# Performance work log

Hardware: AMD Instinct MI355X
Metric: run time of the kernel (lower is better)

The kernel has to match this reference:

```python
import jax, jax.numpy as jnp
import numpy as np

D_MODEL = 1024
D_FF = 4096
NUM_EXPERTS = 8
TOP_K = 2


def setup_inputs() -> dict:
    key = jax.random.key(0)
    ks = jax.random.split(key, 9)
    s = 0.02
    x = jax.random.normal(ks[0], (2, 2048, D_MODEL), dtype=jnp.float32)
    Wg = jax.random.normal(ks[1], (D_MODEL, NUM_EXPERTS), dtype=jnp.float32) * s
    bg = jnp.zeros((NUM_EXPERTS,), dtype=jnp.float32)
    W1 = jax.random.normal(ks[2], (NUM_EXPERTS, D_MODEL, D_FF), dtype=jnp.float32) * s
    b1 = jnp.zeros((NUM_EXPERTS, D_FF), dtype=jnp.float32)
    W3 = jax.random.normal(ks[3], (NUM_EXPERTS, D_MODEL, D_FF), dtype=jnp.float32) * s
    b3 = jnp.zeros((NUM_EXPERTS, D_FF), dtype=jnp.float32)
    W2 = jax.random.normal(ks[4], (NUM_EXPERTS, D_FF, D_MODEL), dtype=jnp.float32) * s
    b2 = jnp.zeros((NUM_EXPERTS, D_MODEL), dtype=jnp.float32)
    return {"x": x, "Wg": Wg, "bg": bg, "W1": W1, "b1": b1,
            "W3": W3, "b3": b3, "W2": W2, "b2": b2}


def reference(x, Wg, bg, W1, b1, W3, b3, W2, b2):
    # Gate (eval mode: no gaussian noise, no dropout)
    logits = x @ Wg + bg                                  # [b, s, E]
    probs = jax.nn.softmax(logits, axis=-1)
    top_v, top_i = jax.lax.top_k(probs, TOP_K)            # [b, s, K]
    top_v = top_v / (top_v.sum(axis=-1, keepdims=True) + 1e-6)
    # combine[b,s,e] = sum_k top_v[b,s,k] * 1[top_i[b,s,k]==e]
    onehot = jax.nn.one_hot(top_i, NUM_EXPERTS, dtype=x.dtype)  # [b, s, K, E]
    combine = jnp.einsum('bsk,bske->bse', top_v, onehot)        # [b, s, E]

    out = jnp.zeros_like(x)
    for e in range(NUM_EXPERTS):
        # SwiGLU expert FFN applied densely; masked-out tokens zeroed by combine weight
        h = jax.nn.silu(x @ W1[e] + b1[e]) * (x @ W3[e] + b3[e])   # [b, s, d_ff]
        out = out + combine[..., e:e + 1] * (h @ W2[e] + b2[e])
    return out
```

## Files before the change

kernel.cpp:

```cpp
#include <hip/hip_runtime.h>
#include <stdint.h>

#define D_MODEL 1024
#define D_FF    4096
#define NE      8
#define T_TOK   4096
#define R_TOT   8192

typedef float f32x4 __attribute__((ext_vector_type(4)));
typedef __bf16 bf16x8 __attribute__((ext_vector_type(8)));
typedef unsigned short ushort_t;

__device__ __forceinline__ ushort_t f2bf(float f) {
    unsigned int u = __float_as_uint(f);
    u += 0x7FFFu + ((u >> 16) & 1u);
    return (ushort_t)(u >> 16);
}

__device__ __forceinline__ void async16(const void* g, const void* l) {
    __builtin_amdgcn_global_load_lds(
        (const __attribute__((address_space(1))) unsigned int*)(uintptr_t)g,
        (__attribute__((address_space(3))) unsigned int*)(uintptr_t)l,
        16, 0, 0);
}

__global__ __launch_bounds__(256) void k_gate(
    const float* __restrict__ x, const float* __restrict__ Wg, const float* __restrict__ bg,
    int* __restrict__ topi, float* __restrict__ topw, int* __restrict__ counts)
{
    int wave = threadIdx.x >> 6, lane = threadIdx.x & 63;
    int t = blockIdx.x * 4 + wave;
    const float* xr = x + (size_t)t * D_MODEL;
    float acc[NE];
#pragma unroll
    for (int e = 0; e < NE; ++e) acc[e] = 0.f;
#pragma unroll
    for (int i = 0; i < D_MODEL / 64; ++i) {
        int k = i * 64 + lane;
        float xv = xr[k];
        const float4* wgp = (const float4*)(Wg + (size_t)k * NE);
        float4 w0 = wgp[0], w1 = wgp[1];
        acc[0] += xv * w0.x; acc[1] += xv * w0.y; acc[2] += xv * w0.z; acc[3] += xv * w0.w;
        acc[4] += xv * w1.x; acc[5] += xv * w1.y; acc[6] += xv * w1.z; acc[7] += xv * w1.w;
    }
#pragma unroll
    for (int off = 32; off >= 1; off >>= 1)
#pragma unroll
        for (int e = 0; e < NE; ++e) acc[e] += __shfl_down(acc[e], off, 64);
    if (lane == 0) {
        float l[NE], m = -1e30f;
#pragma unroll
        for (int e = 0; e < NE; ++e) { l[e] = acc[e] + bg[e]; m = fmaxf(m, l[e]); }
        float p[NE], Z = 0.f;
#pragma unroll
        for (int e = 0; e < NE; ++e) { p[e] = __expf(l[e] - m); Z += p[e]; }
        float invZ = 1.f / Z;
        int i0 = 0; float v0 = -1.f;
#pragma unroll
        for (int e = 0; e < NE; ++e) { p[e] *= invZ; if (p[e] > v0) { v0 = p[e]; i0 = e; } }
        int i1 = 0; float v1 = -1.f;
#pragma unroll
        for (int e = 0; e < NE; ++e) { if (e != i0 && p[e] > v1) { v1 = p[e]; i1 = e; } }
        float denom = 1.f / (v0 + v1 + 1e-6f);
        topi[t * 2 + 0] = i0; topi[t * 2 + 1] = i1;
        topw[t * 2 + 0] = v0 * denom; topw[t * 2 + 1] = v1 * denom;
        atomicAdd(&counts[i0], 1); atomicAdd(&counts[i1], 1);
    }
}

__global__ void k_scan(const int* __restrict__ counts, int* __restrict__ offsets,
                       int* __restrict__ cursors)
{
    if (threadIdx.x == 0) {
        int acc = 0;
        for (int e = 0; e < NE; ++e) { offsets[e] = acc; cursors[e] = acc; acc += counts[e]; }
    }
}

__global__ __launch_bounds__(256) void k_scatter(
    const int* __restrict__ topi, const float* __restrict__ topw,
    int* __restrict__ cursors, int* __restrict__ btok, float* __restrict__ bw)
{
    int t = blockIdx.x * 256 + threadIdx.x;
#pragma unroll
    for (int k = 0; k < 2; ++k) {
        int e = topi[t * 2 + k];
        int p = atomicAdd(&cursors[e], 1);
        btok[p] = t;
        bw[p] = topw[t * 2 + k];
    }
}

__global__ __launch_bounds__(256) void k_gather(
    const float* __restrict__ x, const int* __restrict__ btok, ushort_t* __restrict__ Xg)
{
    int i = blockIdx.x;
    int t = btok[i];
    float4 v = ((const float4*)(x + (size_t)t * D_MODEL))[threadIdx.x];
    ushort4 o;
    o.x = f2bf(v.x); o.y = f2bf(v.y); o.z = f2bf(v.z); o.w = f2bf(v.w);
    ((ushort4*)(Xg + (size_t)i * D_MODEL))[threadIdx.x] = o;
}

__global__ __launch_bounds__(256) void k_transpose(
    const float* __restrict__ W, ushort_t* __restrict__ Wt, int K, int N)
{
    __shared__ ushort_t tile[64 * 72];
    int e = blockIdx.z;
    const float* We = W + (size_t)e * K * N;
    ushort_t* Wte = Wt + (size_t)e * K * N;
    int nb = blockIdx.x * 64, kb = blockIdx.y * 64;
    int tn4 = (threadIdx.x & 15) * 4;
    int tk = threadIdx.x >> 4;
#pragma unroll
    for (int r = 0; r < 4; ++r) {
        int k = r * 16 + tk;
        float4 v = *(const float4*)(We + (size_t)(kb + k) * N + nb + tn4);
        tile[(tn4 + 0) * 72 + k] = f2bf(v.x);
        tile[(tn4 + 1) * 72 + k] = f2bf(v.y);
        tile[(tn4 + 2) * 72 + k] = f2bf(v.z);
        tile[(tn4 + 3) * 72 + k] = f2bf(v.w);
    }
    __syncthreads();
#pragma unroll
    for (int c = 0; c < 4; ++c) {
        int chunk = c * 256 + threadIdx.x;
        int n = chunk >> 4, kc = (chunk & 15) * 4;
        ushort4 o = *(const ushort4*)&tile[n * 72 + kc];
        *(ushort4*)(Wte + (size_t)(nb + n) * K + kb + kc) = o;
    }
}


__global__ __launch_bounds__(512, 2) void k_gemm1(
    const ushort_t* __restrict__ Xg, const ushort_t* __restrict__ W1t,
    const ushort_t* __restrict__ W3t,
    const float* __restrict__ b1, const float* __restrict__ b3,
    const int* __restrict__ counts, const int* __restrict__ offsets,
    ushort_t* __restrict__ H)
{
    __shared__ __align__(16) ushort_t sA [2][256 * 64];
    __shared__ __align__(16) ushort_t sB1[2][128 * 64];
    __shared__ __align__(16) ushort_t sB3[2][128 * 64];

    int bx = blockIdx.x;
    int lx = (bx & 7) * 5 + (bx >> 3);

    int tm = lx, e = 0, cnt = 0;
    for (; e < NE; ++e) {
        cnt = counts[e];
        int nt = (cnt + 255) >> 8;
        if (tm < nt) break;
        tm -= nt;
    }
    if (e >= NE) return;
    int row0 = offsets[e] + tm * 256;
    int rows_left = cnt - tm * 256;

    int tile_n = blockIdx.y * 128;
    int tid = threadIdx.x, wave = tid >> 6, lane = tid & 63;
    int wm = (wave >> 1) * 64, wn = (wave & 1) * 64;
    int col = lane & 15, quad = lane >> 4;

    const ushort_t* W1e = W1t + (size_t)e * D_FF * D_MODEL;
    const ushort_t* W3e = W3t + (size_t)e * D_FF * D_MODEL;

    const ushort_t* gA[4]; const ushort_t* gB1[2]; const ushort_t* gB3[2];
    unsigned offA[4], offB[2];
#pragma unroll
    for (int s = 0; s < 4; ++s) {
        int q = (wave * 4 + s) * 64 + lane;
        int r = q >> 3;
        int cg = ((q & 7) ^ (r & 7)) * 8;
        gA[s]  = Xg + (size_t)(row0 + r) * D_MODEL + cg;
        offA[s] = (unsigned)(wave * 4 + s) * 512;
    }
#pragma unroll
    for (int s = 0; s < 2; ++s) {
        int q = (wave * 2 + s) * 64 + lane;
        int r = q >> 3;
        int cg = ((q & 7) ^ (r & 7)) * 8;
        gB1[s] = W1e + (size_t)(tile_n + r) * D_MODEL + cg;
        gB3[s] = W3e + (size_t)(tile_n + r) * D_MODEL + cg;
        offB[s] = (unsigned)(wave * 2 + s) * 512;
    }

    int swz = (quad ^ (col & 7)) * 8;
    unsigned fA[4], fB[4];
#pragma unroll
    for (int i = 0; i < 4; ++i) {
        fA[i] = (unsigned)(wm + i * 16 + col) * 64 + swz;
        fB[i] = (unsigned)(wn + i * 16 + col) * 64 + swz;
    }

    f32x4 acc1[4][4], acc3[4][4];
#pragma unroll
    for (int i = 0; i < 4; ++i)
#pragma unroll
        for (int j = 0; j < 4; ++j) {
            acc1[i][j] = (f32x4){0.f, 0.f, 0.f, 0.f};
            acc3[i][j] = (f32x4){0.f, 0.f, 0.f, 0.f};
        }

#define STAGE1(p, k0)                                                          \
    do {                                                                       \
        _Pragma("unroll")                                                      \
        for (int s_ = 0; s_ < 4; ++s_) async16(gA[s_] + (k0), &sA[p][offA[s_]]); \
        _Pragma("unroll")                                                      \
        for (int s_ = 0; s_ < 2; ++s_) {                                       \
            async16(gB1[s_] + (k0), &sB1[p][offB[s_]]);                        \
            async16(gB3[s_] + (k0), &sB3[p][offB[s_]]);                        \
        }                                                                      \
    } while (0)

    STAGE1(0, 0);
    for (int t = 0; t < D_MODEL / 64; ++t) {
        int p = t & 1;
        if (t < D_MODEL / 64 - 1) {
            STAGE1(p ^ 1, (t + 1) * 64);
            asm volatile("s_waitcnt vmcnt(8)" ::: "memory");
        } else {
            asm volatile("s_waitcnt vmcnt(0)" ::: "memory");
        }
        __builtin_amdgcn_s_barrier();
        asm volatile("" ::: "memory");
#pragma unroll
        for (int kk = 0; kk < 2; ++kk) {
            unsigned kx = kk * 32;
            bf16x8 a[4], u1[4], u3[4];
#pragma unroll
            for (int j = 0; j < 4; ++j) {
                u1[j] = *(const bf16x8*)(&sB1[p][fB[j] ^ kx]);
                u3[j] = *(const bf16x8*)(&sB3[p][fB[j] ^ kx]);
            }
#pragma unroll
            for (int i = 0; i < 4; ++i) a[i] = *(const bf16x8*)(&sA[p][fA[i] ^ kx]);
            __builtin_amdgcn_s_setprio(1);
#pragma unroll
            for (int i = 0; i < 4; ++i)
#pragma unroll
                for (int j = 0; j < 4; ++j) {
                    acc1[i][j] = __builtin_amdgcn_mfma_f32_16x16x32_bf16(a[i], u1[j], acc1[i][j], 0, 0, 0);
                    acc3[i][j] = __builtin_amdgcn_mfma_f32_16x16x32_bf16(a[i], u3[j], acc3[i][j], 0, 0, 0);
                }
            __builtin_amdgcn_s_setprio(0);
        }
        asm volatile("" ::: "memory");
        __builtin_amdgcn_s_barrier();
        asm volatile("" ::: "memory");
    }
#undef STAGE1

#pragma unroll
    for (int j = 0; j < 4; ++j) {
        int n = tile_n + wn + j * 16 + col;
        float bias1 = b1[e * D_FF + n];
        float bias3 = b3[e * D_FF + n];
#pragma unroll
        for (int i = 0; i < 4; ++i) {
            int rbase = wm + i * 16 + quad * 4;
#pragma unroll
            for (int r = 0; r < 4; ++r) {
                int row = rbase + r;
                if (row < rows_left) {
                    float h1 = acc1[i][j][r] + bias1;
                    float h3 = acc3[i][j][r] + bias3;
                    float s = h1 / (1.f + __expf(-h1));
                    H[(size_t)(row0 + row) * D_FF + n] = f2bf(s * h3);
                }
            }
        }
    }
}

__global__ __launch_bounds__(512, 2) void k_gemm2(
    const ushort_t* __restrict__ H, const ushort_t* __restrict__ W2t,
    const float* __restrict__ b2,
    const int* __restrict__ counts, const int* __restrict__ offsets,
    const int* __restrict__ btok, const float* __restrict__ bw,
    float* __restrict__ out)
{
    __shared__ __align__(16) ushort_t sA[2][256 * 64];
    __shared__ __align__(16) ushort_t sB[2][128 * 64];

    int bx = blockIdx.x;
    int lx = (bx & 7) * 5 + (bx >> 3);

    int tm = lx, e = 0, cnt = 0;
    for (; e < NE; ++e) {
        cnt = counts[e];
        int nt = (cnt + 255) >> 8;
        if (tm < nt) break;
        tm -= nt;
    }
    if (e >= NE) return;
    int row0 = offsets[e] + tm * 256;
    int rows_left = cnt - tm * 256;

    int tile_n = blockIdx.y * 128;
    int tid = threadIdx.x, wave = tid >> 6, lane = tid & 63;
    int wm = (wave >> 1) * 64, wn = (wave & 1) * 64;
    int col = lane & 15, quad = lane >> 4;

    const ushort_t* W2e = W2t + (size_t)e * D_MODEL * D_FF;

    const ushort_t* gA[4]; const ushort_t* gB[2];
    unsigned offA[4], offB[2];
#pragma unroll
    for (int s = 0; s < 4; ++s) {
        int q = (wave * 4 + s) * 64 + lane;
        int r = q >> 3;
        int cg = ((q & 7) ^ (r & 7)) * 8;
        gA[s] = H + (size_t)(row0 + r) * D_FF + cg;
        offA[s] = (unsigned)(wave * 4 + s) * 512;
    }
#pragma unroll
    for (int s = 0; s < 2; ++s) {
        int q = (wave * 2 + s) * 64 + lane;
        int r = q >> 3;
        int cg = ((q & 7) ^ (r & 7)) * 8;
        gB[s] = W2e + (size_t)(tile_n + r) * D_FF + cg;
        offB[s] = (unsigned)(wave * 2 + s) * 512;
    }

    int swz = (quad ^ (col & 7)) * 8;
    unsigned fA[4], fB[4];
#pragma unroll
    for (int i = 0; i < 4; ++i) {
        fA[i] = (unsigned)(wm + i * 16 + col) * 64 + swz;
        fB[i] = (unsigned)(wn + i * 16 + col) * 64 + swz;
    }

    f32x4 acc[4][4];
#pragma unroll
    for (int i = 0; i < 4; ++i)
#pragma unroll
        for (int j = 0; j < 4; ++j) acc[i][j] = (f32x4){0.f, 0.f, 0.f, 0.f};

#define STAGE2(p, k0)                                                          \
    do {                                                                       \
        _Pragma("unroll")                                                      \
        for (int s_ = 0; s_ < 4; ++s_) async16(gA[s_] + (k0), &sA[p][offA[s_]]); \
        _Pragma("unroll")                                                      \
        for (int s_ = 0; s_ < 2; ++s_) async16(gB[s_] + (k0), &sB[p][offB[s_]]); \
    } while (0)

    STAGE2(0, 0);
    for (int t = 0; t < D_FF / 64; ++t) {
        int p = t & 1;
        if (t < D_FF / 64 - 1) {
            STAGE2(p ^ 1, (t + 1) * 64);
            asm volatile("s_waitcnt vmcnt(6)" ::: "memory");
        } else {
            asm volatile("s_waitcnt vmcnt(0)" ::: "memory");
        }
        __builtin_amdgcn_s_barrier();
        asm volatile("" ::: "memory");
#pragma unroll
        for (int kk = 0; kk < 2; ++kk) {
            unsigned kx = kk * 32;
            bf16x8 a[4], b[4];
#pragma unroll
            for (int j = 0; j < 4; ++j) b[j] = *(const bf16x8*)(&sB[p][fB[j] ^ kx]);
#pragma unroll
            for (int i = 0; i < 4; ++i) a[i] = *(const bf16x8*)(&sA[p][fA[i] ^ kx]);
            __builtin_amdgcn_s_setprio(1);
#pragma unroll
            for (int i = 0; i < 4; ++i)
#pragma unroll
                for (int j = 0; j < 4; ++j)
                    acc[i][j] = __builtin_amdgcn_mfma_f32_16x16x32_bf16(a[i], b[j], acc[i][j], 0, 0, 0);
            __builtin_amdgcn_s_setprio(0);
        }
        asm volatile("" ::: "memory");
        __builtin_amdgcn_s_barrier();
        asm volatile("" ::: "memory");
    }
#undef STAGE2

    float bias[4];
#pragma unroll
    for (int j = 0; j < 4; ++j) bias[j] = b2[e * D_MODEL + tile_n + wn + j * 16 + col];

#pragma unroll
    for (int i = 0; i < 4; ++i) {
        int rbase = wm + i * 16 + quad * 4;
#pragma unroll
        for (int r = 0; r < 4; ++r) {
            int row = rbase + r;
            if (row < rows_left) {
                int g_r = row0 + row;
                int t = btok[g_r];
                float w = bw[g_r];
                float* orow = out + (size_t)t * D_MODEL + tile_n + wn + col;
#pragma unroll
                for (int j = 0; j < 4; ++j)
                    atomicAdd(orow + j * 16, w * (acc[i][j][r] + bias[j]));
            }
        }
    }
}

extern "C" void kernel_launch(void* const* d_in, const int* in_sizes, int n_in,
                              void* d_out, int out_size, void* d_ws, size_t ws_size,
                              hipStream_t stream)
{
    const float* x  = (const float*)d_in[0];
    const float* Wg = (const float*)d_in[1];
    const float* bg = (const float*)d_in[2];
    const float* W1 = (const float*)d_in[3];
    const float* b1 = (const float*)d_in[4];
    const float* W3 = (const float*)d_in[5];
    const float* b3 = (const float*)d_in[6];
    const float* W2 = (const float*)d_in[7];
    const float* b2 = (const float*)d_in[8];
    float* out = (float*)d_out;

    char* ws = (char*)d_ws;
    int*   counts  = (int*)(ws + 0);
    int*   cursors = (int*)(ws + 32);
    int*   offsets = (int*)(ws + 64);
    int*   topi    = (int*)(ws + 256);
    float* topw    = (float*)(ws + 256 + 32768);
    int*   btok    = (int*)(ws + 256 + 65536);
    float* bw      = (float*)(ws + 256 + 98304);
    char* p = ws + 131328;
    ushort_t* Xg  = (ushort_t*)p;  p += (size_t)R_TOT * D_MODEL * 2;
    ushort_t* Hb  = (ushort_t*)p;  p += (size_t)R_TOT * D_FF * 2;
    ushort_t* W1t = (ushort_t*)p;  p += (size_t)NE * D_FF * D_MODEL * 2;
    ushort_t* W3t = (ushort_t*)p;  p += (size_t)NE * D_FF * D_MODEL * 2;
    ushort_t* W2t = (ushort_t*)p;

    hipMemsetAsync(ws, 0, 64, stream);
    hipMemsetAsync(d_out, 0, (size_t)out_size * 4, stream);

    k_gate<<<dim3(T_TOK / 4), dim3(256), 0, stream>>>(x, Wg, bg, topi, topw, counts);
    k_scan<<<dim3(1), dim3(64), 0, stream>>>(counts, offsets, cursors);
    k_scatter<<<dim3(T_TOK / 256), dim3(256), 0, stream>>>(topi, topw, cursors, btok, bw);
    k_gather<<<dim3(R_TOT), dim3(256), 0, stream>>>(x, btok, Xg);
    k_transpose<<<dim3(D_FF / 64, D_MODEL / 64, NE), dim3(256), 0, stream>>>(W1, W1t, D_MODEL, D_FF);
    k_transpose<<<dim3(D_FF / 64, D_MODEL / 64, NE), dim3(256), 0, stream>>>(W3, W3t, D_MODEL, D_FF);
    k_transpose<<<dim3(D_MODEL / 64, D_FF / 64, NE), dim3(256), 0, stream>>>(W2, W2t, D_FF, D_MODEL);
    k_gemm1<<<dim3(40, D_FF / 128), dim3(512), 0, stream>>>(Xg, W1t, W3t, b1, b3, counts, offsets, Hb);
    k_gemm2<<<dim3(40, D_MODEL / 128), dim3(512), 0, stream>>>(Hb, W2t, b2, counts, offsets, btok, bw, out);
}
```

Before: 914.6 us.

## Interleave prefetch with MFMA phases, triple-buffer gemm2, replace atomics with combine kernel

The gemm1 main loop is split into four half-K MFMA phases. Each phase issues part of the next tile's async loads, so global-to-LDS traffic overlaps with compute instead of arriving in one burst. gemm2 moves to a three-stage LDS buffer with prefetch two tiles ahead, and now writes unweighted per-slot outputs to a scratch buffer Y (aliased onto W1t) instead of doing float atomicAdds into out. A new k_combine kernel gathers the two expert rows per token using positions recorded by k_scatter. This removes the output memset and atomic contention, at the cost of more barriers, more LDS per block (possible occupancy loss) and an extra pass over Y.

```diff
diff --git a/kernel.cpp b/kernel.cpp
--- a/kernel.cpp
+++ b/kernel.cpp
@@ -23,6 +23,8 @@
         (__attribute__((address_space(3))) unsigned int*)(uintptr_t)l,
         16, 0, 0);
 }
+
+#define FENCE() asm volatile("" ::: "memory")
 
 __global__ __launch_bounds__(256) void k_gate(
     const float* __restrict__ x, const float* __restrict__ Wg, const float* __restrict__ bg,
@@ -78,16 +80,18 @@
 }
 
 __global__ __launch_bounds__(256) void k_scatter(
-    const int* __restrict__ topi, const float* __restrict__ topw,
+    const int* __restrict__ topi_in, const float* __restrict__ topw,
     int* __restrict__ cursors, int* __restrict__ btok, float* __restrict__ bw)
 {
     int t = blockIdx.x * 256 + threadIdx.x;
+    int* topi = (int*)topi_in;
 #pragma unroll
     for (int k = 0; k < 2; ++k) {
         int e = topi[t * 2 + k];
         int p = atomicAdd(&cursors[e], 1);
         btok[p] = t;
         bw[p] = topw[t * 2 + k];
+        topi[t * 2 + k] = p;
     }
 }
 
@@ -202,54 +206,106 @@
             acc3[i][j] = (f32x4){0.f, 0.f, 0.f, 0.f};
         }
 
-#define STAGE1(p, k0)                                                          \
-    do {                                                                       \
-        _Pragma("unroll")                                                      \
-        for (int s_ = 0; s_ < 4; ++s_) async16(gA[s_] + (k0), &sA[p][offA[s_]]); \
-        _Pragma("unroll")                                                      \
-        for (int s_ = 0; s_ < 2; ++s_) {                                       \
-            async16(gB1[s_] + (k0), &sB1[p][offB[s_]]);                        \
-            async16(gB3[s_] + (k0), &sB3[p][offB[s_]]);                        \
-        }                                                                      \
-    } while (0)
-
-    STAGE1(0, 0);
+#pragma unroll
+    for (int s = 0; s < 4; ++s) async16(gA[s], &sA[0][offA[s]]);
+#pragma unroll
+    for (int s = 0; s < 2; ++s) async16(gB1[s], &sB1[0][offB[s]]);
+#pragma unroll
+    for (int s = 0; s < 2; ++s) async16(gB3[s], &sB3[0][offB[s]]);
+    asm volatile("s_waitcnt vmcnt(2)" ::: "memory");
+    __builtin_amdgcn_s_barrier();
+    FENCE();
+
     for (int t = 0; t < D_MODEL / 64; ++t) {
         int p = t & 1;
-        if (t < D_MODEL / 64 - 1) {
-            STAGE1(p ^ 1, (t + 1) * 64);
-            asm volatile("s_waitcnt vmcnt(8)" ::: "memory");
+        int k1 = (t + 1) * 64;
+        bool pf = (t < D_MODEL / 64 - 1);
+        bf16x8 a[4], u[4];
+
+#pragma unroll
+        for (int i = 0; i < 4; ++i) a[i] = *(const bf16x8*)(&sA[p][fA[i]]);
+#pragma unroll
+        for (int j = 0; j < 4; ++j) u[j] = *(const bf16x8*)(&sB1[p][fB[j]]);
+        if (pf) {
+            async16(gA[0] + k1, &sA[p ^ 1][offA[0]]);
+            async16(gA[1] + k1, &sA[p ^ 1][offA[1]]);
+            asm volatile("s_waitcnt vmcnt(2)" ::: "memory");
         } else {
             asm volatile("s_waitcnt vmcnt(0)" ::: "memory");
         }
         __builtin_amdgcn_s_barrier();
-        asm volatile("" ::: "memory");
-#pragma unroll
-        for (int kk = 0; kk < 2; ++kk) {
-            unsigned kx = kk * 32;
-            bf16x8 a[4], u1[4], u3[4];
-#pragma unroll
-            for (int j = 0; j < 4; ++j) {
-                u1[j] = *(const bf16x8*)(&sB1[p][fB[j] ^ kx]);
-                u3[j] = *(const bf16x8*)(&sB3[p][fB[j] ^ kx]);
-            }
-#pragma unroll
-            for (int i = 0; i < 4; ++i) a[i] = *(const bf16x8*)(&sA[p][fA[i] ^ kx]);
-            __builtin_amdgcn_s_setprio(1);
-#pragma unroll
-            for (int i = 0; i < 4; ++i)
-#pragma unroll
-                for (int j = 0; j < 4; ++j) {
-                    acc1[i][j] = __builtin_amdgcn_mfma_f32_16x16x32_bf16(a[i], u1[j], acc1[i][j], 0, 0, 0);
-                    acc3[i][j] = __builtin_amdgcn_mfma_f32_16x16x32_bf16(a[i], u3[j], acc3[i][j], 0, 0, 0);
-                }
-            __builtin_amdgcn_s_setprio(0);
-        }
-        asm volatile("" ::: "memory");
-        __builtin_amdgcn_s_barrier();
-        asm volatile("" ::: "memory");
-    }
-#undef STAGE1
+        FENCE();
+        __builtin_amdgcn_s_setprio(1);
+#pragma unroll
+        for (int i = 0; i < 4; ++i)
+#pragma unroll
+            for (int j = 0; j < 4; ++j)
+                acc1[i][j] = __builtin_amdgcn_mfma_f32_16x16x32_bf16(a[i], u[j], acc1[i][j], 0, 0, 0);
+        __builtin_amdgcn_s_setprio(0);
+        FENCE();
+        __builtin_amdgcn_s_barrier();
+        FENCE();
+
+#pragma unroll
+        for (int j = 0; j < 4; ++j) u[j] = *(const bf16x8*)(&sB3[p][fB[j]]);
+        if (pf) {
+            async16(gA[2] + k1, &sA[p ^ 1][offA[2]]);
+            async16(gA[3] + k1, &sA[p ^ 1][offA[3]]);
+        }
+        __builtin_amdgcn_s_barrier();
+        FENCE();
+        __builtin_amdgcn_s_setprio(1);
+#pragma unroll
+        for (int i = 0; i < 4; ++i)
+#pragma unroll
+            for (int j = 0; j < 4; ++j)
+                acc3[i][j] = __builtin_amdgcn_mfma_f32_16x16x32_bf16(a[i], u[j], acc3[i][j], 0, 0, 0);
+        __builtin_amdgcn_s_setprio(0);
+        FENCE();
+        __builtin_amdgcn_s_barrier();
+        FENCE();
+
+#pragma unroll
+        for (int i = 0; i < 4; ++i) a[i] = *(const bf16x8*)(&sA[p][fA[i] ^ 32]);
+#pragma unroll
+        for (int j = 0; j < 4; ++j) u[j] = *(const bf16x8*)(&sB1[p][fB[j] ^ 32]);
+        if (pf) {
+            async16(gB1[0] + k1, &sB1[p ^ 1][offB[0]]);
+            async16(gB1[1] + k1, &sB1[p ^ 1][offB[1]]);
+        }
+        __builtin_amdgcn_s_barrier();
+        FENCE();
+        __builtin_amdgcn_s_setprio(1);
+#pragma unroll
+        for (int i = 0; i < 4; ++i)
+#pragma unroll
+            for (int j = 0; j < 4; ++j)
+                acc1[i][j] = __builtin_amdgcn_mfma_f32_16x16x32_bf16(a[i], u[j], acc1[i][j], 0, 0, 0);
+        __builtin_amdgcn_s_setprio(0);
+        FENCE();
+        __builtin_amdgcn_s_barrier();
+        FENCE();
+
+#pragma unroll
+        for (int j = 0; j < 4; ++j) u[j] = *(const bf16x8*)(&sB3[p][fB[j] ^ 32]);
+        if (pf) {
+            async16(gB3[0] + k1, &sB3[p ^ 1][offB[0]]);
+            async16(gB3[1] + k1, &sB3[p ^ 1][offB[1]]);
+            asm volatile("s_waitcnt vmcnt(2)" ::: "memory");
+        }
+        __builtin_amdgcn_s_barrier();
+        FENCE();
+        __builtin_amdgcn_s_setprio(1);
+#pragma unroll
+        for (int i = 0; i < 4; ++i)
+#pragma unroll
+            for (int j = 0; j < 4; ++j)
+                acc3[i][j] = __builtin_amdgcn_mfma_f32_16x16x32_bf16(a[i], u[j], acc3[i][j], 0, 0, 0);
+        __builtin_amdgcn_s_setprio(0);
+        FENCE();
+        __builtin_amdgcn_s_barrier();
+        FENCE();
+    }
 
 #pragma unroll
     for (int j = 0; j < 4; ++j) {
@@ -277,11 +333,10 @@
     const ushort_t* __restrict__ H, const ushort_t* __restrict__ W2t,
     const float* __restrict__ b2,
     const int* __restrict__ counts, const int* __restrict__ offsets,
-    const int* __restrict__ btok, const float* __restrict__ bw,
-    float* __restrict__ out)
-{
-    __shared__ __align__(16) ushort_t sA[2][256 * 64];
-    __shared__ __align__(16) ushort_t sB[2][128 * 64];
+    float* __restrict__ Y)
+{
+    __shared__ __align__(16) ushort_t sA[3][256 * 64];
+    __shared__ __align__(16) ushort_t sB[3][128 * 64];
 
     int bx = blockIdx.x;
     int lx = (bx & 7) * 5 + (bx >> 3);
@@ -337,46 +392,74 @@
 #pragma unroll
         for (int j = 0; j < 4; ++j) acc[i][j] = (f32x4){0.f, 0.f, 0.f, 0.f};
 
-#define STAGE2(p, k0)                                                          \
-    do {                                                                       \
-        _Pragma("unroll")                                                      \
-        for (int s_ = 0; s_ < 4; ++s_) async16(gA[s_] + (k0), &sA[p][offA[s_]]); \
-        _Pragma("unroll")                                                      \
-        for (int s_ = 0; s_ < 2; ++s_) async16(gB[s_] + (k0), &sB[p][offB[s_]]); \
-    } while (0)
-
-    STAGE2(0, 0);
+#pragma unroll
+    for (int s = 0; s < 4; ++s) async16(gA[s], &sA[0][offA[s]]);
+#pragma unroll
+    for (int s = 0; s < 2; ++s) async16(gB[s], &sB[0][offB[s]]);
+#pragma unroll
+    for (int s = 0; s < 4; ++s) async16(gA[s] + 64, &sA[1][offA[s]]);
+#pragma unroll
+    for (int s = 0; s < 2; ++s) async16(gB[s] + 64, &sB[1][offB[s]]);
+    asm volatile("s_waitcnt vmcnt(6)" ::: "memory");
+    __builtin_amdgcn_s_barrier();
+    FENCE();
+
+    int pb = 0;
     for (int t = 0; t < D_FF / 64; ++t) {
-        int p = t & 1;
-        if (t < D_FF / 64 - 1) {
-            STAGE2(p ^ 1, (t + 1) * 64);
+        int pn = (pb == 0) ? 2 : pb - 1;
+        int k2 = (t + 2) * 64;
+        bool pf = (t < D_FF / 64 - 2);
+        bf16x8 a[4], b[4];
+
+#pragma unroll
+        for (int i = 0; i < 4; ++i) a[i] = *(const bf16x8*)(&sA[pb][fA[i]]);
+#pragma unroll
+        for (int j = 0; j < 4; ++j) b[j] = *(const bf16x8*)(&sB[pb][fB[j]]);
+        if (pf) {
+            async16(gA[0] + k2, &sA[pn][offA[0]]);
+            async16(gA[1] + k2, &sA[pn][offA[1]]);
+            async16(gA[2] + k2, &sA[pn][offA[2]]);
+        }
+        __builtin_amdgcn_s_barrier();
+        FENCE();
+        __builtin_amdgcn_s_setprio(1);
+#pragma unroll
+        for (int i = 0; i < 4; ++i)
+#pragma unroll
+            for (int j = 0; j < 4; ++j)
+                acc[i][j] = __builtin_amdgcn_mfma_f32_16x16x32_bf16(a[i], b[j], acc[i][j], 0, 0, 0);
+        __builtin_amdgcn_s_setprio(0);
+        FENCE();
+        __builtin_amdgcn_s_barrier();
+        FENCE();
+
+#pragma unroll
+        for (int i = 0; i < 4; ++i) a[i] = *(const bf16x8*)(&sA[pb][fA[i] ^ 32]);
+#pragma unroll
+        for (int j = 0; j < 4; ++j) b[j] = *(const bf16x8*)(&sB[pb][fB[j] ^ 32]);
+        if (pf) {
+            async16(gA[3] + k2, &sA[pn][offA[3]]);
+            async16(gB[0] + k2, &sB[pn][offB[0]]);
+            async16(gB[1] + k2, &sB[pn][offB[1]]);
             asm volatile("s_waitcnt vmcnt(6)" ::: "memory");
         } else {
             asm volatile("s_waitcnt vmcnt(0)" ::: "memory");
         }
         __builtin_amdgcn_s_barrier();
-        asm volatile("" ::: "memory");
-#pragma unroll
-        for (int kk = 0; kk < 2; ++kk) {
-            unsigned kx = kk * 32;
-            bf16x8 a[4], b[4];
-#pragma unroll
-            for (int j = 0; j < 4; ++j) b[j] = *(const bf16x8*)(&sB[p][fB[j] ^ kx]);
-#pragma unroll
-            for (int i = 0; i < 4; ++i) a[i] = *(const bf16x8*)(&sA[p][fA[i] ^ kx]);
-            __builtin_amdgcn_s_setprio(1);
-#pragma unroll
-            for (int i = 0; i < 4; ++i)
-#pragma unroll
-                for (int j = 0; j < 4; ++j)
-                    acc[i][j] = __builtin_amdgcn_mfma_f32_16x16x32_bf16(a[i], b[j], acc[i][j], 0, 0, 0);
-            __builtin_amdgcn_s_setprio(0);
-        }
-        asm volatile("" ::: "memory");
-        __builtin_amdgcn_s_barrier();
-        asm volatile("" ::: "memory");
-    }
-#undef STAGE2
+        FENCE();
+        __builtin_amdgcn_s_setprio(1);
+#pragma unroll
+        for (int i = 0; i < 4; ++i)
+#pragma unroll
+            for (int j = 0; j < 4; ++j)
+                acc[i][j] = __builtin_amdgcn_mfma_f32_16x16x32_bf16(a[i], b[j], acc[i][j], 0, 0, 0);
+        __builtin_amdgcn_s_setprio(0);
+        FENCE();
+        __builtin_amdgcn_s_barrier();
+        FENCE();
+
+        pb = (pb == 2) ? 0 : pb + 1;
+    }
 
     float bias[4];
 #pragma unroll
@@ -389,16 +472,30 @@
         for (int r = 0; r < 4; ++r) {
             int row = rbase + r;
             if (row < rows_left) {
-                int g_r = row0 + row;
-                int t = btok[g_r];
-                float w = bw[g_r];
-                float* orow = out + (size_t)t * D_MODEL + tile_n + wn + col;
+                float* yrow = Y + (size_t)(row0 + row) * D_MODEL + tile_n + wn + col;
 #pragma unroll
                 for (int j = 0; j < 4; ++j)
-                    atomicAdd(orow + j * 16, w * (acc[i][j][r] + bias[j]));
+                    yrow[j * 16] = acc[i][j][r] + bias[j];
             }
         }
     }
+}
+
+__global__ __launch_bounds__(256) void k_combine(
+    const float* __restrict__ Y, const int* __restrict__ pos,
+    const float* __restrict__ topw, float* __restrict__ out)
+{
+    int t = blockIdx.x, c = threadIdx.x;
+    int p0 = pos[t * 2 + 0], p1 = pos[t * 2 + 1];
+    float w0 = topw[t * 2 + 0], w1 = topw[t * 2 + 1];
+    float4 y0 = ((const float4*)(Y + (size_t)p0 * D_MODEL))[c];
+    float4 y1 = ((const float4*)(Y + (size_t)p1 * D_MODEL))[c];
+    float4 o;
+    o.x = w0 * y0.x + w1 * y1.x;
+    o.y = w0 * y0.y + w1 * y1.y;
+    o.z = w0 * y0.z + w1 * y1.z;
+    o.w = w0 * y0.w + w1 * y1.w;
+    ((float4*)(out + (size_t)t * D_MODEL))[c] = o;
 }
 
 extern "C" void kernel_launch(void* const* d_in, const int* in_sizes, int n_in,
@@ -430,9 +527,9 @@
     ushort_t* W1t = (ushort_t*)p;  p += (size_t)NE * D_FF * D_MODEL * 2;
     ushort_t* W3t = (ushort_t*)p;  p += (size_t)NE * D_FF * D_MODEL * 2;
     ushort_t* W2t = (ushort_t*)p;
+    float* Y = (float*)W1t;
 
     hipMemsetAsync(ws, 0, 64, stream);
-    hipMemsetAsync(d_out, 0, (size_t)out_size * 4, stream);
 
     k_gate<<<dim3(T_TOK / 4), dim3(256), 0, stream>>>(x, Wg, bg, topi, topw, counts);
     k_scan<<<dim3(1), dim3(64), 0, stream>>>(counts, offsets, cursors);
@@ -442,5 +539,6 @@
     k_transpose<<<dim3(D_FF / 64, D_MODEL / 64, NE), dim3(256), 0, stream>>>(W3, W3t, D_MODEL, D_FF);
     k_transpose<<<dim3(D_MODEL / 64, D_FF / 64, NE), dim3(256), 0, stream>>>(W2, W2t, D_FF, D_MODEL);
     k_gemm1<<<dim3(40, D_FF / 128), dim3(512), 0, stream>>>(Xg, W1t, W3t, b1, b3, counts, offsets, Hb);
-    k_gemm2<<<dim3(40, D_MODEL / 128), dim3(512), 0, stream>>>(Hb, W2t, b2, counts, offsets, btok, bw, out);
-}
+    k_gemm2<<<dim3(40, D_MODEL / 128), dim3(512), 0, stream>>>(Hb, W2t, b2, counts, offsets, Y);
+    k_combine<<<dim3(T_TOK), dim3(256), 0, stream>>>(Y, topi, topw, out);
+}
```

After: 894.2 us. 1.02x faster.

## Shrink GEMM tiles to 128x128x32 and replace atomic scatter with combine kernel

Applied to the files above, without the earlier changes.

Both expert GEMMs move from 256x128 tiles with 512 threads and K-step 64 to 128x128 tiles with 256 threads and K-step 32, with a new LDS swizzle and more blocks. This aims for better load balance and occupancy across CUs. The second GEMM now writes per-slot outputs to a buffer (reusing the W1t region), and a new combine kernel forms the weighted sum of each token's two expert rows. This removes the float atomics and the output memset. It costs an extra read and write of an 8192x1024 float buffer, and halving the tiles doubles global operand traffic per FLOP.

```diff
diff --git a/kernel.cpp b/kernel.cpp
--- a/kernel.cpp
+++ b/kernel.cpp
@@ -78,16 +78,18 @@
 }
 
 __global__ __launch_bounds__(256) void k_scatter(
-    const int* __restrict__ topi, const float* __restrict__ topw,
+    const int* __restrict__ topi_in, const float* __restrict__ topw,
     int* __restrict__ cursors, int* __restrict__ btok, float* __restrict__ bw)
 {
     int t = blockIdx.x * 256 + threadIdx.x;
+    int* topi = (int*)topi_in;
 #pragma unroll
     for (int k = 0; k < 2; ++k) {
         int e = topi[t * 2 + k];
         int p = atomicAdd(&cursors[e], 1);
         btok[p] = t;
         bw[p] = topw[t * 2 + k];
+        topi[t * 2 + k] = p;
     }
 }
 
@@ -105,7 +107,7 @@
 __global__ __launch_bounds__(256) void k_transpose(
     const float* __restrict__ W, ushort_t* __restrict__ Wt, int K, int N)
 {
-    __shared__ ushort_t tile[64 * 72];
+    __shared__ ushort_t tile[64 * 76];
     int e = blockIdx.z;
     const float* We = W + (size_t)e * K * N;
     ushort_t* Wte = Wt + (size_t)e * K * N;
@@ -116,46 +118,46 @@
     for (int r = 0; r < 4; ++r) {
         int k = r * 16 + tk;
         float4 v = *(const float4*)(We + (size_t)(kb + k) * N + nb + tn4);
-        tile[(tn4 + 0) * 72 + k] = f2bf(v.x);
-        tile[(tn4 + 1) * 72 + k] = f2bf(v.y);
-        tile[(tn4 + 2) * 72 + k] = f2bf(v.z);
-        tile[(tn4 + 3) * 72 + k] = f2bf(v.w);
+        tile[(tn4 + 0) * 76 + k] = f2bf(v.x);
+        tile[(tn4 + 1) * 76 + k] = f2bf(v.y);
+        tile[(tn4 + 2) * 76 + k] = f2bf(v.z);
+        tile[(tn4 + 3) * 76 + k] = f2bf(v.w);
     }
     __syncthreads();
 #pragma unroll
     for (int c = 0; c < 4; ++c) {
         int chunk = c * 256 + threadIdx.x;
         int n = chunk >> 4, kc = (chunk & 15) * 4;
-        ushort4 o = *(const ushort4*)&tile[n * 72 + kc];
+        ushort4 o = *(const ushort4*)&tile[n * 76 + kc];
         *(ushort4*)(Wte + (size_t)(nb + n) * K + kb + kc) = o;
     }
 }
 
 
-__global__ __launch_bounds__(512, 2) void k_gemm1(
+__global__ __launch_bounds__(256, 2) void k_gemm1(
     const ushort_t* __restrict__ Xg, const ushort_t* __restrict__ W1t,
     const ushort_t* __restrict__ W3t,
     const float* __restrict__ b1, const float* __restrict__ b3,
     const int* __restrict__ counts, const int* __restrict__ offsets,
     ushort_t* __restrict__ H)
 {
-    __shared__ __align__(16) ushort_t sA [2][256 * 64];
-    __shared__ __align__(16) ushort_t sB1[2][128 * 64];
-    __shared__ __align__(16) ushort_t sB3[2][128 * 64];
+    __shared__ __align__(16) ushort_t sA [2][128 * 32];
+    __shared__ __align__(16) ushort_t sB1[2][128 * 32];
+    __shared__ __align__(16) ushort_t sB3[2][128 * 32];
 
     int bx = blockIdx.x;
-    int lx = (bx & 7) * 5 + (bx >> 3);
+    int lx = (bx & 7) * 9 + (bx >> 3);
 
     int tm = lx, e = 0, cnt = 0;
     for (; e < NE; ++e) {
         cnt = counts[e];
-        int nt = (cnt + 255) >> 8;
+        int nt = (cnt + 127) >> 7;
         if (tm < nt) break;
         tm -= nt;
     }
     if (e >= NE) return;
-    int row0 = offsets[e] + tm * 256;
-    int rows_left = cnt - tm * 256;
+    int row0 = offsets[e] + tm * 128;
+    int rows_left = cnt - tm * 128;
 
     int tile_n = blockIdx.y * 128;
     int tid = threadIdx.x, wave = tid >> 6, lane = tid & 63;
@@ -165,32 +167,27 @@
     const ushort_t* W1e = W1t + (size_t)e * D_FF * D_MODEL;
     const ushort_t* W3e = W3t + (size_t)e * D_FF * D_MODEL;
 
-    const ushort_t* gA[4]; const ushort_t* gB1[2]; const ushort_t* gB3[2];
-    unsigned offA[4], offB[2];
-#pragma unroll
-    for (int s = 0; s < 4; ++s) {
-        int q = (wave * 4 + s) * 64 + lane;
-        int r = q >> 3;
-        int cg = ((q & 7) ^ (r & 7)) * 8;
-        gA[s]  = Xg + (size_t)(row0 + r) * D_MODEL + cg;
-        offA[s] = (unsigned)(wave * 4 + s) * 512;
-    }
+    const ushort_t* gA[2]; const ushort_t* gB1[2]; const ushort_t* gB3[2];
+    unsigned ldsOff[2];
 #pragma unroll
     for (int s = 0; s < 2; ++s) {
-        int q = (wave * 2 + s) * 64 + lane;
-        int r = q >> 3;
-        int cg = ((q & 7) ^ (r & 7)) * 8;
+        int u = wave * 2 + s;
+        int q = u * 64 + lane;
+        int r = q >> 2;
+        int cg = ((q & 3) ^ ((r >> 1) & 3)) * 8;
+        gA[s]  = Xg  + (size_t)(row0 + r) * D_MODEL + cg;
         gB1[s] = W1e + (size_t)(tile_n + r) * D_MODEL + cg;
         gB3[s] = W3e + (size_t)(tile_n + r) * D_MODEL + cg;
-        offB[s] = (unsigned)(wave * 2 + s) * 512;
-    }
-
-    int swz = (quad ^ (col & 7)) * 8;
+        ldsOff[s] = (unsigned)u * 512;
+    }
+
     unsigned fA[4], fB[4];
 #pragma unroll
     for (int i = 0; i < 4; ++i) {
-        fA[i] = (unsigned)(wm + i * 16 + col) * 64 + swz;
-        fB[i] = (unsigned)(wn + i * 16 + col) * 64 + swz;
+        int ra = wm + i * 16 + col;
+        int rb = wn + i * 16 + col;
+        fA[i] = (unsigned)ra * 32 + ((quad ^ ((ra >> 1) & 3)) * 8);
+        fB[i] = (unsigned)rb * 32 + ((quad ^ ((rb >> 1) & 3)) * 8);
     }
 
     f32x4 acc1[4][4], acc3[4][4];
@@ -202,49 +199,49 @@
             acc3[i][j] = (f32x4){0.f, 0.f, 0.f, 0.f};
         }
 
-#define STAGE1(p, k0)                                                          \
-    do {                                                                       \
-        _Pragma("unroll")                                                      \
-        for (int s_ = 0; s_ < 4; ++s_) async16(gA[s_] + (k0), &sA[p][offA[s_]]); \
-        _Pragma("unroll")                                                      \
-        for (int s_ = 0; s_ < 2; ++s_) {                                       \
-            async16(gB1[s_] + (k0), &sB1[p][offB[s_]]);                        \
-            async16(gB3[s_] + (k0), &sB3[p][offB[s_]]);                        \
-        }                                                                      \
+#define STAGE1(p, k0)                                                            \
+    do {                                                                         \
+        _Pragma("unroll")                                                        \
+        for (int s_ = 0; s_ < 2; ++s_) {                                         \
+            async16(gA[s_]  + (k0), &sA [p][ldsOff[s_]]);                        \
+            async16(gB1[s_] + (k0), &sB1[p][ldsOff[s_]]);                        \
+            async16(gB3[s_] + (k0), &sB3[p][ldsOff[s_]]);                        \
+        }                                                                        \
     } while (0)
 
     STAGE1(0, 0);
-    for (int t = 0; t < D_MODEL / 64; ++t) {
+    for (int t = 0; t < D_MODEL / 32; ++t) {
         int p = t & 1;
-        if (t < D_MODEL / 64 - 1) {
-            STAGE1(p ^ 1, (t + 1) * 64);
-            asm volatile("s_waitcnt vmcnt(8)" ::: "memory");
+        if (t < D_MODEL / 32 - 1) {
+            STAGE1(p ^ 1, (t + 1) * 32);
+            asm volatile("s_waitcnt vmcnt(6)" ::: "memory");
         } else {
             asm volatile("s_waitcnt vmcnt(0)" ::: "memory");
         }
         __builtin_amdgcn_s_barrier();
         asm volatile("" ::: "memory");
-#pragma unroll
-        for (int kk = 0; kk < 2; ++kk) {
-            unsigned kx = kk * 32;
-            bf16x8 a[4], u1[4], u3[4];
-#pragma unroll
-            for (int j = 0; j < 4; ++j) {
-                u1[j] = *(const bf16x8*)(&sB1[p][fB[j] ^ kx]);
-                u3[j] = *(const bf16x8*)(&sB3[p][fB[j] ^ kx]);
-            }
-#pragma unroll
-            for (int i = 0; i < 4; ++i) a[i] = *(const bf16x8*)(&sA[p][fA[i] ^ kx]);
-            __builtin_amdgcn_s_setprio(1);
-#pragma unroll
-            for (int i = 0; i < 4; ++i)
-#pragma unroll
-                for (int j = 0; j < 4; ++j) {
-                    acc1[i][j] = __builtin_amdgcn_mfma_f32_16x16x32_bf16(a[i], u1[j], acc1[i][j], 0, 0, 0);
-                    acc3[i][j] = __builtin_amdgcn_mfma_f32_16x16x32_bf16(a[i], u3[j], acc3[i][j], 0, 0, 0);
-                }
-            __builtin_amdgcn_s_setprio(0);
-        }
+
+        bf16x8 a[4], u[4];
+#pragma unroll
+        for (int i = 0; i < 4; ++i) a[i] = *(const bf16x8*)(&sA[p][fA[i]]);
+#pragma unroll
+        for (int j = 0; j < 4; ++j) u[j] = *(const bf16x8*)(&sB1[p][fB[j]]);
+        __builtin_amdgcn_s_setprio(1);
+#pragma unroll
+        for (int i = 0; i < 4; ++i)
+#pragma unroll
+            for (int j = 0; j < 4; ++j)
+                acc1[i][j] = __builtin_amdgcn_mfma_f32_16x16x32_bf16(a[i], u[j], acc1[i][j], 0, 0, 0);
+        __builtin_amdgcn_s_setprio(0);
+#pragma unroll
+        for (int j = 0; j < 4; ++j) u[j] = *(const bf16x8*)(&sB3[p][fB[j]]);
+        __builtin_amdgcn_s_setprio(1);
+#pragma unroll
+        for (int i = 0; i < 4; ++i)
+#pragma unroll
+            for (int j = 0; j < 4; ++j)
+                acc3[i][j] = __builtin_amdgcn_mfma_f32_16x16x32_bf16(a[i], u[j], acc3[i][j], 0, 0, 0);
+        __builtin_amdgcn_s_setprio(0);
         asm volatile("" ::: "memory");
         __builtin_amdgcn_s_barrier();
         asm volatile("" ::: "memory");
@@ -273,29 +270,28 @@
     }
 }
 
-__global__ __launch_bounds__(512, 2) void k_gemm2(
+__global__ __launch_bounds__(256, 4) void k_gemm2(
     const ushort_t* __restrict__ H, const ushort_t* __restrict__ W2t,
     const float* __restrict__ b2,
     const int* __restrict__ counts, const int* __restrict__ offsets,
-    const int* __restrict__ btok, const float* __restrict__ bw,
-    float* __restrict__ out)
-{
-    __shared__ __align__(16) ushort_t sA[2][256 * 64];
-    __shared__ __align__(16) ushort_t sB[2][128 * 64];
+    float* __restrict__ Y)
+{
+    __shared__ __align__(16) ushort_t sA[2][128 * 32];
+    __shared__ __align__(16) ushort_t sB[2][128 * 32];
 
     int bx = blockIdx.x;
-    int lx = (bx & 7) * 5 + (bx >> 3);
+    int lx = (bx & 7) * 9 + (bx >> 3);
 
     int tm = lx, e = 0, cnt = 0;
     for (; e < NE; ++e) {
         cnt = counts[e];
-        int nt = (cnt + 255) >> 8;
+        int nt = (cnt + 127) >> 7;
         if (tm < nt) break;
         tm -= nt;
     }
     if (e >= NE) return;
-    int row0 = offsets[e] + tm * 256;
-    int rows_left = cnt - tm * 256;
+    int row0 = offsets[e] + tm * 128;
+    int rows_left = cnt - tm * 128;
 
     int tile_n = blockIdx.y * 128;
     int tid = threadIdx.x, wave = tid >> 6, lane = tid & 63;
@@ -304,31 +300,26 @@
 
     const ushort_t* W2e = W2t + (size_t)e * D_MODEL * D_FF;
 
-    const ushort_t* gA[4]; const ushort_t* gB[2];
-    unsigned offA[4], offB[2];
-#pragma unroll
-    for (int s = 0; s < 4; ++s) {
-        int q = (wave * 4 + s) * 64 + lane;
-        int r = q >> 3;
-        int cg = ((q & 7) ^ (r & 7)) * 8;
-        gA[s] = H + (size_t)(row0 + r) * D_FF + cg;
-        offA[s] = (unsigned)(wave * 4 + s) * 512;
-    }
+    const ushort_t* gA[2]; const ushort_t* gB[2];
+    unsigned ldsOff[2];
 #pragma unroll
     for (int s = 0; s < 2; ++s) {
-        int q = (wave * 2 + s) * 64 + lane;
-        int r = q >> 3;
-        int cg = ((q & 7) ^ (r & 7)) * 8;
+        int u = wave * 2 + s;
+        int q = u * 64 + lane;
+        int r = q >> 2;
+        int cg = ((q & 3) ^ ((r >> 1) & 3)) * 8;
+        gA[s] = H   + (size_t)(row0 + r) * D_FF + cg;
         gB[s] = W2e + (size_t)(tile_n + r) * D_FF + cg;
-        offB[s] = (unsigned)(wave * 2 + s) * 512;
-    }
-
-    int swz = (quad ^ (col & 7)) * 8;
+        ldsOff[s] = (unsigned)u * 512;
+    }
+
     unsigned fA[4], fB[4];
 #pragma unroll
     for (int i = 0; i < 4; ++i) {
-        fA[i] = (unsigned)(wm + i * 16 + col) * 64 + swz;
-        fB[i] = (unsigned)(wn + i * 16 + col) * 64 + swz;
+        int ra = wm + i * 16 + col;
+        int rb = wn + i * 16 + col;
+        fA[i] = (unsigned)ra * 32 + ((quad ^ ((ra >> 1) & 3)) * 8);
+        fB[i] = (unsigned)rb * 32 + ((quad ^ ((rb >> 1) & 3)) * 8);
     }
 
     f32x4 acc[4][4];
@@ -337,41 +328,39 @@
 #pragma unroll
         for (int j = 0; j < 4; ++j) acc[i][j] = (f32x4){0.f, 0.f, 0.f, 0.f};
 
-#define STAGE2(p, k0)                                                          \
-    do {                                                                       \
-        _Pragma("unroll")                                                      \
-        for (int s_ = 0; s_ < 4; ++s_) async16(gA[s_] + (k0), &sA[p][offA[s_]]); \
-        _Pragma("unroll")                                                      \
-        for (int s_ = 0; s_ < 2; ++s_) async16(gB[s_] + (k0), &sB[p][offB[s_]]); \
+#define STAGE2(p, k0)                                                            \
+    do {                                                                         \
+        _Pragma("unroll")                                                        \
+        for (int s_ = 0; s_ < 2; ++s_) {                                         \
+            async16(gA[s_] + (k0), &sA[p][ldsOff[s_]]);                          \
+            async16(gB[s_] + (k0), &sB[p][ldsOff[s_]]);                          \
+        }                                                                        \
     } while (0)
 
     STAGE2(0, 0);
-    for (int t = 0; t < D_FF / 64; ++t) {
+    for (int t = 0; t < D_FF / 32; ++t) {
         int p = t & 1;
-        if (t < D_FF / 64 - 1) {
-            STAGE2(p ^ 1, (t + 1) * 64);
-            asm volatile("s_waitcnt vmcnt(6)" ::: "memory");
+        if (t < D_FF / 32 - 1) {
+            STAGE2(p ^ 1, (t + 1) * 32);
+            asm volatile("s_waitcnt vmcnt(4)" ::: "memory");
         } else {
             asm volatile("s_waitcnt vmcnt(0)" ::: "memory");
         }
         __builtin_amdgcn_s_barrier();
         asm volatile("" ::: "memory");
-#pragma unroll
-        for (int kk = 0; kk < 2; ++kk) {
-            unsigned kx = kk * 32;
-            bf16x8 a[4], b[4];
-#pragma unroll
-            for (int j = 0; j < 4; ++j) b[j] = *(const bf16x8*)(&sB[p][fB[j] ^ kx]);
-#pragma unroll
-            for (int i = 0; i < 4; ++i) a[i] = *(const bf16x8*)(&sA[p][fA[i] ^ kx]);
-            __builtin_amdgcn_s_setprio(1);
-#pragma unroll
-            for (int i = 0; i < 4; ++i)
-#pragma unroll
-                for (int j = 0; j < 4; ++j)
-                    acc[i][j] = __builtin_amdgcn_mfma_f32_16x16x32_bf16(a[i], b[j], acc[i][j], 0, 0, 0);
-            __builtin_amdgcn_s_setprio(0);
-        }
+
+        bf16x8 a[4], b[4];
+#pragma unroll
+        for (int i = 0; i < 4; ++i) a[i] = *(const bf16x8*)(&sA[p][fA[i]]);
+#pragma unroll
+        for (int j = 0; j < 4; ++j) b[j] = *(const bf16x8*)(&sB[p][fB[j]]);
+        __builtin_amdgcn_s_setprio(1);
+#pragma unroll
+        for (int i = 0; i < 4; ++i)
+#pragma unroll
+            for (int j = 0; j < 4; ++j)
+                acc[i][j] = __builtin_amdgcn_mfma_f32_16x16x32_bf16(a[i], b[j], acc[i][j], 0, 0, 0);
+        __builtin_amdgcn_s_setprio(0);
         asm volatile("" ::: "memory");
         __builtin_amdgcn_s_barrier();
         asm volatile("" ::: "memory");
@@ -389,16 +378,30 @@
         for (int r = 0; r < 4; ++r) {
             int row = rbase + r;
             if (row < rows_left) {
-                int g_r = row0 + row;
-                int t = btok[g_r];
-                float w = bw[g_r];
-                float* orow = out + (size_t)t * D_MODEL + tile_n + wn + col;
+                float* yrow = Y + (size_t)(row0 + row) * D_MODEL + tile_n + wn + col;
 #pragma unroll
                 for (int j = 0; j < 4; ++j)
-                    atomicAdd(orow + j * 16, w * (acc[i][j][r] + bias[j]));
+                    yrow[j * 16] = acc[i][j][r] + bias[j];
             }
         }
     }
+}
+
+__global__ __launch_bounds__(256) void k_combine(
+    const float* __restrict__ Y, const int* __restrict__ pos,
+    const float* __restrict__ topw, float* __restrict__ out)
+{
+    int t = blockIdx.x, c = threadIdx.x;
+    int p0 = pos[t * 2 + 0], p1 = pos[t * 2 + 1];
+    float w0 = topw[t * 2 + 0], w1 = topw[t * 2 + 1];
+    float4 y0 = ((const float4*)(Y + (size_t)p0 * D_MODEL))[c];
+    float4 y1 = ((const float4*)(Y + (size_t)p1 * D_MODEL))[c];
+    float4 o;
+    o.x = w0 * y0.x + w1 * y1.x;
+    o.y = w0 * y0.y + w1 * y1.y;
+    o.z = w0 * y0.z + w1 * y1.z;
+    o.w = w0 * y0.w + w1 * y1.w;
+    ((float4*)(out + (size_t)t * D_MODEL))[c] = o;
 }
 
 extern "C" void kernel_launch(void* const* d_in, const int* in_sizes, int n_in,
@@ -430,9 +433,9 @@
     ushort_t* W1t = (ushort_t*)p;  p += (size_t)NE * D_FF * D_MODEL * 2;
     ushort_t* W3t = (ushort_t*)p;  p += (size_t)NE * D_FF * D_MODEL * 2;
     ushort_t* W2t = (ushort_t*)p;
+    float* Y = (float*)W1t;
 
     hipMemsetAsync(ws, 0, 64, stream);
-    hipMemsetAsync(d_out, 0, (size_t)out_size * 4, stream);
 
     k_gate<<<dim3(T_TOK / 4), dim3(256), 0, stream>>>(x, Wg, bg, topi, topw, counts);
     k_scan<<<dim3(1), dim3(64), 0, stream>>>(counts, offsets, cursors);
@@ -441,6 +444,7 @@
     k_transpose<<<dim3(D_FF / 64, D_MODEL / 64, NE), dim3(256), 0, stream>>>(W1, W1t, D_MODEL, D_FF);
     k_transpose<<<dim3(D_FF / 64, D_MODEL / 64, NE), dim3(256), 0, stream>>>(W3, W3t, D_MODEL, D_FF);
     k_transpose<<<dim3(D_MODEL / 64, D_FF / 64, NE), dim3(256), 0, stream>>>(W2, W2t, D_FF, D_MODEL);
-    k_gemm1<<<dim3(40, D_FF / 128), dim3(512), 0, stream>>>(Xg, W1t, W3t, b1, b3, counts, offsets, Hb);
-    k_gemm2<<<dim3(40, D_MODEL / 128), dim3(512), 0, stream>>>(Hb, W2t, b2, counts, offsets, btok, bw, out);
-}
+    k_gemm1<<<dim3(72, D_FF / 128), dim3(256), 0, stream>>>(Xg, W1t, W3t, b1, b3, counts, offsets, Hb);
+    k_gemm2<<<dim3(72, D_MODEL / 128), dim3(256), 0, stream>>>(Hb, W2t, b2, counts, offsets, Y);
+    k_combine<<<dim3(T_TOK), dim3(256), 0, stream>>>(Y, topi, topw, out);
+}
```

Result: no change. 911.2 us (-0.4%).
